# Kernel optimization log

Hardware: AMD Instinct MI355X
Metric: run time of the kernel (lower is better)

The kernel has to match this reference:

```python
import jax, jax.numpy as jnp
import numpy as np
from jax import lax

PATCH = 8

def setup_inputs() -> dict:
    key = jax.random.key(0)
    ks = jax.random.split(key, 5)
    x = jax.random.normal(ks[0], (4, 64, 256, 256), dtype=jnp.float32)
    w_in = jax.random.normal(ks[1], (512, 64), dtype=jnp.float32) * 0.02
    b_in = jnp.zeros((512,), dtype=jnp.float32)
    w_dw = jax.random.normal(ks[2], (512, 1, 3, 3), dtype=jnp.float32) * 0.02
    b_dw = jnp.zeros((512,), dtype=jnp.float32)
    w_out = jax.random.normal(ks[3], (64, 256), dtype=jnp.float32) * 0.02
    b_out = jnp.zeros((64,), dtype=jnp.float32)
    fft_filter = jnp.ones((64, 1, 1, PATCH, PATCH // 2 + 1), dtype=jnp.float32)
    return {"x": x, "w_in": w_in, "b_in": b_in, "w_dw": w_dw, "b_dw": b_dw,
            "w_out": w_out, "b_out": b_out, "fft_filter": fft_filter}

def reference(x, w_in, b_in, w_dw, b_dw, w_out, b_out, fft_filter):
    # project_in: 1x1 conv == channel GEMM. x: [B, C, H, W] -> [B, 2h, H, W]
    h = jnp.einsum('oc,bchw->bohw', w_in, x) + b_in[None, :, None, None]
    # depthwise 3x3 conv, padding=1
    h = lax.conv_general_dilated(
        h, w_dw, window_strides=(1, 1), padding='SAME',
        dimension_numbers=('NCHW', 'OIHW', 'NCHW'),
        feature_group_count=w_dw.shape[0]) + b_dw[None, :, None, None]
    x1, x2 = jnp.split(h, 2, axis=1)
    h = jax.nn.gelu(x1, approximate=False) * x2  # exact GELU like F.gelu
    # project_out: 1x1 conv
    y = jnp.einsum('oc,bchw->bohw', w_out, h) + b_out[None, :, None, None]
    # patch-wise spectral filtering
    B, C, H, W = y.shape
    p = PATCH
    yp = y.reshape(B, C, H // p, p, W // p, p).transpose(0, 1, 2, 4, 3, 5)  # b c h w p1 p2
    yf = jnp.fft.rfft2(yp)              # b c h w p1 (p2//2+1)
    yf = yf * fft_filter                # filter broadcasts over (c,1,1,p1,p2r)
    yp = jnp.fft.irfft2(yf, s=(p, p))
    y = yp.transpose(0, 1, 2, 4, 3, 5).reshape(B, C, H, W)
    return y
```

## Files before the change

### kernel.cpp

```cpp
#include <hip/hip_runtime.h>
#include <math.h>

typedef __attribute__((ext_vector_type(8))) short short8;
typedef __attribute__((ext_vector_type(4))) float f32x4;
typedef __attribute__((ext_vector_type(2))) float f32x2;
typedef _Float16 f16x8 __attribute__((ext_vector_type(8)));

#define TILE 16
#define IH 256
#define IW 256

#define WSA_OFF 16384
#define WSC_OFF 81920

#define H_STRIDE 1456
#define H_BUF 23296
#define G_OFF 46592
#define G_BUF 16384
#define SMEM_BYTES 79360

__device__ __forceinline__ unsigned short f2bf(float f) {
  unsigned int u = __builtin_bit_cast(unsigned int, f);
  u = (u + 0x7FFFu + ((u >> 16) & 1u)) >> 16;
  return (unsigned short)u;
}

__global__ void edffn_prep(const float* __restrict__ fftf,
                           const float* __restrict__ w_in,
                           const float* __restrict__ w_out,
                           float* __restrict__ ws) {
  int blk = blockIdx.x, t = threadIdx.x;
  if (blk < 64) {
    int a = t >> 3, bb = t & 7;
    const float c0 = 0.70710678118654752f;
    const float ctab[8] = {1.f, c0, 0.f, -c0, -1.f, -c0, 0.f, c0};
    const float* F = fftf + blk * 40;
    float acc = 0.f;
    for (int k1 = 0; k1 < 8; ++k1)
      for (int k2 = 0; k2 < 8; ++k2) {
        float f = (k2 <= 4) ? F[k1 * 5 + k2] : F[((8 - k1) & 7) * 5 + (8 - k2)];
        acc += f * ctab[(k1 * a + k2 * bb) & 7];
      }
    ws[blk * 64 + t] = acc * (1.f / 64.f);
  } else if (blk < 128) {
    int b2 = blk - 64;
    int q = b2 >> 2, s = (b2 >> 1) & 1, ks = b2 & 1;
    int row = (s ? 256 : 0) + q * 16 + (t & 15);
    unsigned short* dst =
        (unsigned short*)((unsigned char*)ws + WSA_OFF) + (((q * 2 + s) * 2 + ks) * 64 + t) * 8;
    for (int j = 0; j < 8; ++j) {
      int k = ks * 32 + (t >> 4) * 8 + j;
      dst[j] = f2bf(w_in[row * 64 + k]);
    }
  } else {
    int b3 = blk - 128;
    int p = b3 >> 2, mt = b3 & 3;
    int row = mt * 16 + (t & 15);
    unsigned short* dst =
        (unsigned short*)((unsigned char*)ws + WSC_OFF) + ((p * 4 + mt) * 64 + t) * 8;
    for (int j = 0; j < 8; ++j) {
      int k = p * 32 + (t >> 4) * 8 + j;
      _Float16 hv = (_Float16)w_out[row * 256 + k];
      dst[j] = __builtin_bit_cast(unsigned short, hv);
    }
  }
}

__global__ __launch_bounds__(256, 2) void edffn_main(
    const float* __restrict__ x, const float* __restrict__ b_in,
    const float* __restrict__ w_dw, const float* __restrict__ b_dw,
    const float* __restrict__ b_out, const float* __restrict__ ws,
    float* __restrict__ out) {
  __shared__ __align__(16) unsigned char smem[SMEM_BYTES];
  __shared__ int s_flag;
  const int t = threadIdx.x;
  const int lane = t & 63, wave = t >> 6;
  const int l15 = lane & 15, lg = lane >> 4;
  const int gx0 = blockIdx.x * TILE, gy0 = blockIdx.y * TILE;
  const int b = blockIdx.z;
  const unsigned short* wsA = (const unsigned short*)((const unsigned char*)ws + WSA_OFF);
  const unsigned short* wsC = (const unsigned short*)((const unsigned char*)ws + WSC_OFF);

  short8 xf[6][2];
  int haddr[6];
  unsigned vmask = 0, imask = 0;
  const float* xb = x + (size_t)b * 64 * 65536;
#pragma unroll
  for (int i = 0; i < 6; ++i) {
    int nt = wave + 4 * i;
    int n = nt * 16 + l15;
    int hy = n / 18;
    int hx = n - hy * 18;
    int gy = gy0 + hy - 1, gx = gx0 + hx - 1;
    int vnt = (nt < 21) & (n < 324);
    int inb = vnt & (gy >= 0) & (gy < IH) & (gx >= 0) & (gx < IW);
    haddr[i] = hy * 80 + hx * 4;
    vmask |= (unsigned)vnt << i;
    imask |= (unsigned)inb << i;
    int gyc = min(max(gy, 0), IH - 1), gxc = min(max(gx, 0), IW - 1);
    const float* xp = xb + (size_t)gyc * IW + gxc;
#pragma unroll
    for (int ks = 0; ks < 2; ++ks) {
#pragma unroll
      for (int j = 0; j < 8; ++j) {
        int k = ks * 32 + lg * 8 + j;
        unsigned short bf = f2bf(xp[(size_t)k * 65536]);
        xf[i][ks][j] = (short)(inb ? bf : (unsigned short)0);
      }
    }
  }

  f32x4 accY[16];
#pragma unroll
  for (int i = 0; i < 16; ++i) accY[i] = (f32x4){0.f, 0.f, 0.f, 0.f};

  const int cp_dw = t & 15;
  const int oy_dw = t >> 4;

  auto loadWD = [&](int qq, unsigned (&wd)[9], unsigned& bd) {
    const int cg1 = qq * 16 + cp_dw, cg2 = 256 + qq * 16 + cp_dw;
#pragma unroll
    for (int u = 0; u < 9; ++u) {
      float w1 = w_dw[cg1 * 9 + u], w2 = w_dw[cg2 * 9 + u];
      asm("v_cvt_pkrtz_f16_f32 %0, %1, %2" : "=v"(wd[u]) : "v"(w1), "v"(w2));
    }
    float b1 = b_dw[cg1], b2 = b_dw[cg2];
    asm("v_cvt_pkrtz_f16_f32 %0, %1, %2" : "=v"(bd) : "v"(b1), "v"(b2));
  };

  auto stageA = [&](int qq) {
    short8 af[2][2];
#pragma unroll
    for (int s = 0; s < 2; ++s)
#pragma unroll
      for (int ks = 0; ks < 2; ++ks)
        af[s][ks] = *(const short8*)(wsA + (((qq * 2 + s) * 2 + ks) * 64 + lane) * 8);
    float bin[2][4];
#pragma unroll
    for (int s = 0; s < 2; ++s)
#pragma unroll
      for (int r = 0; r < 4; ++r) bin[s][r] = b_in[(s ? 256 : 0) + qq * 16 + lg * 4 + r];
    unsigned char* Hb = smem + (qq & 1) * H_BUF;
#pragma unroll
    for (int i = 0; i < 6; ++i) {
      if (wave + 4 * i < 21) {
        f32x4 acc0 = {0.f, 0.f, 0.f, 0.f}, acc1 = {0.f, 0.f, 0.f, 0.f};
        acc0 = __builtin_amdgcn_mfma_f32_16x16x32_bf16(af[0][0], xf[i][0], acc0, 0, 0, 0);
        acc0 = __builtin_amdgcn_mfma_f32_16x16x32_bf16(af[0][1], xf[i][1], acc0, 0, 0, 0);
        acc1 = __builtin_amdgcn_mfma_f32_16x16x32_bf16(af[1][0], xf[i][0], acc1, 0, 0, 0);
        acc1 = __builtin_amdgcn_mfma_f32_16x16x32_bf16(af[1][1], xf[i][1], acc1, 0, 0, 0);
        if ((vmask >> i) & 1u) {
          unsigned keep = (imask >> i) & 1u;
#pragma unroll
          for (int r = 0; r < 4; ++r) {
            float v0 = acc0[r] + bin[0][r];
            float v1 = acc1[r] + bin[1][r];
            unsigned pk;
            asm("v_cvt_pkrtz_f16_f32 %0, %1, %2" : "=v"(pk) : "v"(v0), "v"(v1));
            pk = keep ? pk : 0u;
            *(unsigned*)(Hb + (lg * 4 + r) * H_STRIDE + haddr[i]) = pk;
          }
        }
      }
    }
  };

#define PKC(nm, val)                                            \
  unsigned nm;                                                  \
  {                                                             \
    float fv = (val);                                           \
    asm("v_cvt_pkrtz_f16_f32 %0, %1, %1" : "=v"(nm) : "v"(fv)); \
  }
  PKC(kSQ, 0.70710678f)
  PKC(kC216, 1.f / 216.f)
  PKC(kCm42, -1.f / 42.f)
  PKC(kC10, 0.1f)
  PKC(kCm3, -1.f / 3.f)
  PKC(kOne, 1.0f)
  PKC(kHalf, 0.5f)
  PKC(kErf, 1.12837917f)
#undef PKC

  auto dwconv = [&](int qq, const unsigned (&wd)[9], unsigned bd) {
    const int cp = cp_dw, oy = oy_dw;
    const unsigned char* Hb = smem + (qq & 1) * H_BUF;
    unsigned a[16];
#pragma unroll
    for (int j = 0; j < 16; ++j) a[j] = bd;
#pragma unroll
    for (int dy = 0; dy < 3; ++dy) {
      const uint4* rp = (const uint4*)(Hb + cp * H_STRIDE + (oy + dy) * 80);
      uint4 r0 = rp[0], r1 = rp[1], r2 = rp[2], r3 = rp[3];
      uint2 r4 = ((const uint2*)rp)[8];
      unsigned e[18] = {r0.x, r0.y, r0.z, r0.w, r1.x, r1.y, r1.z, r1.w,
                        r2.x, r2.y, r2.z, r2.w, r3.x, r3.y, r3.z, r3.w,
                        r4.x, r4.y};
#pragma unroll
      for (int ox = 0; ox < 16; ++ox) {
#pragma unroll
        for (int dx = 0; dx < 3; ++dx)
          asm("v_pk_fma_f16 %0, %1, %2, %0"
              : "+v"(a[ox])
              : "v"(wd[dy * 3 + dx]), "v"(e[ox + dx]));
      }
    }
    const int c2 = (qq & 1) * 16 + cp;
    const int gi = (c2 >> 3) ^ (oy & 3);
    unsigned short* Gp = (unsigned short*)(smem + G_OFF + ((qq >> 1) & 1) * G_BUF) +
                         oy * 16 * 32 + gi * 8 + (c2 & 7);
    unsigned umax = 0;
    unsigned gw[8];
#pragma unroll
    for (int j = 0; j < 8; ++j) {
      unsigned a0 = a[2 * j], a1 = a[2 * j + 1];
      unsigned u = __builtin_amdgcn_perm(a1, a0, 0x05040100u);
      unsigned v = __builtin_amdgcn_perm(a1, a0, 0x07060302u);
      unsigned uabs = u & 0x7FFF7FFFu;
      asm("v_pk_max_f16 %0, %1, %2" : "=v"(umax) : "v"(umax), "v"(uabs));
      unsigned z, z2, p, erfv, tt, g;
      asm("v_pk_mul_f16 %0, %1, %2" : "=v"(z) : "v"(u), "v"(kSQ));
      asm("v_pk_mul_f16 %0, %1, %2" : "=v"(z2) : "v"(z), "v"(z));
      asm("v_pk_fma_f16 %0, %1, %2, %3" : "=v"(p) : "v"(z2), "v"(kC216), "v"(kCm42));
      asm("v_pk_fma_f16 %0, %1, %2, %3" : "=v"(p) : "v"(z2), "v"(p), "v"(kC10));
      asm("v_pk_fma_f16 %0, %1, %2, %3" : "=v"(p) : "v"(z2), "v"(p), "v"(kCm3));
      asm("v_pk_fma_f16 %0, %1, %2, %3" : "=v"(p) : "v"(z2), "v"(p), "v"(kOne));
      asm("v_pk_mul_f16 %0, %1, %2" : "=v"(erfv) : "v"(z), "v"(p));
      asm("v_pk_mul_f16 %0, %1, %2" : "=v"(erfv) : "v"(erfv), "v"(kErf));
      asm("v_pk_fma_f16 %0, %1, %2, %2" : "=v"(tt) : "v"(erfv), "v"(kHalf));
      asm("v_pk_mul_f16 %0, %1, %2" : "=v"(g) : "v"(u), "v"(tt));
      asm("v_pk_mul_f16 %0, %1, %2" : "=v"(g) : "v"(g), "v"(v));
      gw[j] = g;
    }
    {
      float m0, m1;
      unsigned uh = umax >> 16;
      asm("v_cvt_f32_f16 %0, %1" : "=v"(m0) : "v"(umax));
      asm("v_cvt_f32_f16 %0, %1" : "=v"(m1) : "v"(uh));
      if (__builtin_expect(fmaxf(m0, m1) > 0.565685f, 0)) {
#pragma unroll
        for (int j = 0; j < 8; ++j) {
          float g01[2];
#pragma unroll
          for (int kx = 0; kx < 2; ++kx) {
            unsigned aw = a[2 * j + kx], ah = aw >> 16;
            float hu, hv2;
            asm("v_cvt_f32_f16 %0, %1" : "=v"(hu) : "v"(aw));
            asm("v_cvt_f32_f16 %0, %1" : "=v"(hv2) : "v"(ah));
            g01[kx] = 0.5f * hu * (1.f + erff(hu * 0.70710678f)) * hv2;
          }
          unsigned pk;
          asm("v_cvt_pkrtz_f16_f32 %0, %1, %2" : "=v"(pk) : "v"(g01[0]), "v"(g01[1]));
          gw[j] = pk;
        }
      }
    }
#pragma unroll
    for (int j = 0; j < 8; ++j) {
      Gp[(2 * j) * 32] = (unsigned short)gw[j];
      Gp[(2 * j + 1) * 32] = (unsigned short)(gw[j] >> 16);
    }
  };

  unsigned wdA[9], wdB[9], bdA, bdB;
  f16x8 cfC;

  auto stageC8 = [&](int pc, int nt0) {
    const unsigned short* G = (const unsigned short*)(smem + G_OFF + (pc & 1) * G_BUF);
#pragma unroll
    for (int k = 0; k < 8; ++k) {
      int nt = nt0 + k;
      int g = lg ^ (nt & 3);
      int n = nt * 16 + l15;
      f16x8 bf = *(const f16x8*)(G + n * 32 + g * 8);
      accY[nt] = __builtin_amdgcn_mfma_f32_16x16x32_f16(cfC, bf, accY[nt], 0, 0, 0);
    }
  };

  loadWD(0, wdA, bdA);
  loadWD(1, wdB, bdB);
  cfC = *(const f16x8*)(wsC + ((0 * 4 + wave) * 64 + lane) * 8);
  __builtin_amdgcn_s_setprio(1);
  stageA(0);
  stageA(1);
  __builtin_amdgcn_s_setprio(0);
  __syncthreads();

  for (int p = 0; p < 8; ++p) {
    if (p >= 1) {
      __builtin_amdgcn_s_setprio(1);
      stageC8(p - 1, 0);
      __builtin_amdgcn_s_setprio(0);
    }
    dwconv(2 * p, wdA, bdA);
    if (p >= 1) {
      __builtin_amdgcn_s_setprio(1);
      stageC8(p - 1, 8);
      __builtin_amdgcn_s_setprio(0);
      cfC = *(const f16x8*)(wsC + ((p * 4 + wave) * 64 + lane) * 8);
    }
    dwconv(2 * p + 1, wdB, bdB);
    __syncthreads();

    if (p < 7) {
      __builtin_amdgcn_s_setprio(1);
      stageA(2 * p + 2);
      stageA(2 * p + 3);
      __builtin_amdgcn_s_setprio(0);
      loadWD(2 * p + 2, wdA, bdA);
      loadWD(2 * p + 3, wdB, bdB);
      __syncthreads();
    }
  }

  __builtin_amdgcn_s_setprio(1);
  stageC8(7, 0);
  stageC8(7, 8);
  __builtin_amdgcn_s_setprio(0);

  {
    f32x4 bo;
#pragma unroll
    for (int r = 0; r < 4; ++r) bo[r] = b_out[wave * 16 + lg * 4 + r];
#pragma unroll
    for (int nt = 0; nt < 16; ++nt)
#pragma unroll
      for (int r = 0; r < 4; ++r) accY[nt][r] += bo[r];
  }

  if (t == 0) s_flag = 1;
  __syncthreads();
  {
    int ok = 1;
    const float* kc = ws;
#pragma unroll
    for (int j = 0; j < 16; ++j) {
      int idx = t * 16 + j;
      float e = ((idx & 63) == 0) ? 1.f : 0.f;
      ok &= (fabsf(kc[idx] - e) <= 1e-5f) ? 1 : 0;
    }
    if (!ok) s_flag = 0;
  }
  __syncthreads();

  const int o = wave * 16 + lg * 4;
  if (s_flag) {
#pragma unroll
    for (int nt = 0; nt < 16; ++nt) {
      float* op = out + (((size_t)(b * 64 + o)) * IH + gy0 + nt) * IW + gx0 + l15;
#pragma unroll
      for (int r = 0; r < 4; ++r) op[(size_t)r * IH * IW] = accY[nt][r];
    }
    return;
  }

  float* YS = (float*)smem;
  for (int half = 0; half < 2; ++half) {
    __syncthreads();
    if ((wave >> 1) == half) {
      int c32 = (wave & 1) * 16 + lg * 4;
#pragma unroll
      for (int nt = 0; nt < 16; ++nt)
#pragma unroll
        for (int r = 0; r < 4; ++r) YS[(c32 + r) * 260 + nt * 16 + l15] = accY[nt][r];
    }
    __syncthreads();
    if (t < 128) {
      int o32 = t >> 2, oo = half * 32 + o32, qd = t & 3;
      const float* kp = ws + oo * 64;
      int py0 = (qd >> 1) * 8, px0 = (qd & 1) * 8;
      const float* row = YS + o32 * 260;
      for (int i = 0; i < 8; ++i)
        for (int j = 0; j < 8; ++j) {
          float acc = 0.f;
          for (int a_ = 0; a_ < 8; ++a_)
            for (int b_ = 0; b_ < 8; ++b_)
              acc += kp[a_ * 8 + b_] *
                     row[(py0 + ((i - a_) & 7)) * 16 + px0 + ((j - b_) & 7)];
          out[(((size_t)(b * 64 + oo)) * IH + gy0 + py0 + i) * IW + gx0 + px0 + j] = acc;
        }
    }
  }
}

extern "C" void kernel_launch(void* const* d_in, const int* in_sizes, int n_in,
                              void* d_out, int out_size, void* d_ws, size_t ws_size,
                              hipStream_t stream) {
  const float* x = (const float*)d_in[0];
  const float* w_in = (const float*)d_in[1];
  const float* b_in = (const float*)d_in[2];
  const float* w_dw = (const float*)d_in[3];
  const float* b_dw = (const float*)d_in[4];
  const float* w_out = (const float*)d_in[5];
  const float* b_out = (const float*)d_in[6];
  const float* fftf = (const float*)d_in[7];
  float* out = (float*)d_out;
  float* ws = (float*)d_ws;

  edffn_prep<<<160, 64, 0, stream>>>(fftf, w_in, w_out, ws);
  dim3 grid(IW / TILE, IH / TILE, 4);
  edffn_main<<<grid, 256, 0, stream>>>(x, b_in, w_dw, b_dw, b_out, ws, out);
}
```

Measured before the change: 141.7 us.

## Split fused FFN kernel into two kernels with fp16 intermediate in workspace

Splits the single fused kernel into two. The first runs project-in, depthwise conv and GELU gating, then writes the gated fp16 activations to a global workspace buffer. The second reads them back with double-buffered LDS staging and runs project-out plus the spectral filter. The split lowers shared memory and register pressure per kernel so more blocks fit per CU. In exchange it adds a global round trip of about 134 MB of intermediate data and an extra launch, and falls back to the fused kernel if the workspace is too small.

```diff
diff --git a/kernel.cpp b/kernel.cpp
--- a/kernel.cpp
+++ b/kernel.cpp
@@ -12,12 +12,17 @@
 
 #define WSA_OFF 16384
 #define WSC_OFF 81920
+#define GH_OFF 131072
 
 #define H_STRIDE 1456
 #define H_BUF 23296
 #define G_OFF 46592
 #define G_BUF 16384
 #define SMEM_BYTES 79360
+
+#define K1_G_OFF 23296
+#define K1_SMEM 39680
+#define K2_SMEM 33280
 
 __device__ __forceinline__ unsigned short f2bf(float f) {
   unsigned int u = __builtin_bit_cast(unsigned int, f);
@@ -66,6 +71,13 @@
   }
 }
 
+#define PKC(nm, val)                                            \
+  unsigned nm;                                                  \
+  {                                                             \
+    float fv = (val);                                           \
+    asm("v_cvt_pkrtz_f16_f32 %0, %1, %1" : "=v"(nm) : "v"(fv)); \
+  }
+
 __global__ __launch_bounds__(256, 2) void edffn_main(
     const float* __restrict__ x, const float* __restrict__ b_in,
     const float* __restrict__ w_dw, const float* __restrict__ b_dw,
@@ -165,12 +177,6 @@
     }
   };
 
-#define PKC(nm, val)                                            \
-  unsigned nm;                                                  \
-  {                                                             \
-    float fv = (val);                                           \
-    asm("v_cvt_pkrtz_f16_f32 %0, %1, %1" : "=v"(nm) : "v"(fv)); \
-  }
   PKC(kSQ, 0.70710678f)
   PKC(kC216, 1.f / 216.f)
   PKC(kCm42, -1.f / 42.f)
@@ -179,7 +185,6 @@
   PKC(kOne, 1.0f)
   PKC(kHalf, 0.5f)
   PKC(kErf, 1.12837917f)
-#undef PKC
 
   auto dwconv = [&](int qq, const unsigned (&wd)[9], unsigned bd) {
     const int cp = cp_dw, oy = oy_dw;
@@ -300,7 +305,6 @@
     }
     dwconv(2 * p + 1, wdB, bdB);
     __syncthreads();
-
     if (p < 7) {
       __builtin_amdgcn_s_setprio(1);
       stageA(2 * p + 2);
@@ -382,6 +386,341 @@
   }
 }
 
+__global__ __launch_bounds__(256, 3) void edffn_k1(
+    const float* __restrict__ x, const float* __restrict__ b_in,
+    const float* __restrict__ w_dw, const float* __restrict__ b_dw,
+    const float* __restrict__ ws, unsigned char* __restrict__ Gh) {
+  __shared__ __align__(16) unsigned char smem[K1_SMEM];
+  const int t = threadIdx.x;
+  const int lane = t & 63, wave = t >> 6;
+  const int l15 = lane & 15, lg = lane >> 4;
+  const int gx0 = blockIdx.x * TILE, gy0 = blockIdx.y * TILE;
+  const int b = blockIdx.z;
+  const size_t blkL = ((size_t)b * 16 + blockIdx.y) * 16 + blockIdx.x;
+  const unsigned short* wsA = (const unsigned short*)((const unsigned char*)ws + WSA_OFF);
+
+  short8 xf[6][2];
+  int haddr[6];
+  unsigned vmask = 0, imask = 0;
+  const float* xb = x + (size_t)b * 64 * 65536;
+#pragma unroll
+  for (int i = 0; i < 6; ++i) {
+    int nt = wave + 4 * i;
+    int n = nt * 16 + l15;
+    int hy = n / 18;
+    int hx = n - hy * 18;
+    int gy = gy0 + hy - 1, gx = gx0 + hx - 1;
+    int vnt = (nt < 21) & (n < 324);
+    int inb = vnt & (gy >= 0) & (gy < IH) & (gx >= 0) & (gx < IW);
+    haddr[i] = hy * 80 + hx * 4;
+    vmask |= (unsigned)vnt << i;
+    imask |= (unsigned)inb << i;
+    int gyc = min(max(gy, 0), IH - 1), gxc = min(max(gx, 0), IW - 1);
+    const float* xp = xb + (size_t)gyc * IW + gxc;
+#pragma unroll
+    for (int ks = 0; ks < 2; ++ks) {
+#pragma unroll
+      for (int j = 0; j < 8; ++j) {
+        int k = ks * 32 + lg * 8 + j;
+        unsigned short bf = f2bf(xp[(size_t)k * 65536]);
+        xf[i][ks][j] = (short)(inb ? bf : (unsigned short)0);
+      }
+    }
+  }
+
+  const int cp_dw = t & 15;
+  const int oy_dw = t >> 4;
+
+  auto loadWD = [&](int qq, unsigned (&wd)[9], unsigned& bd) {
+    const int cg1 = qq * 16 + cp_dw, cg2 = 256 + qq * 16 + cp_dw;
+#pragma unroll
+    for (int u = 0; u < 9; ++u) {
+      float w1 = w_dw[cg1 * 9 + u], w2 = w_dw[cg2 * 9 + u];
+      asm("v_cvt_pkrtz_f16_f32 %0, %1, %2" : "=v"(wd[u]) : "v"(w1), "v"(w2));
+    }
+    float b1 = b_dw[cg1], b2 = b_dw[cg2];
+    asm("v_cvt_pkrtz_f16_f32 %0, %1, %2" : "=v"(bd) : "v"(b1), "v"(b2));
+  };
+
+  auto stageA = [&](int qq) {
+    short8 af[2][2];
+#pragma unroll
+    for (int s = 0; s < 2; ++s)
+#pragma unroll
+      for (int ks = 0; ks < 2; ++ks)
+        af[s][ks] = *(const short8*)(wsA + (((qq * 2 + s) * 2 + ks) * 64 + lane) * 8);
+    float bin[2][4];
+#pragma unroll
+    for (int s = 0; s < 2; ++s)
+#pragma unroll
+      for (int r = 0; r < 4; ++r) bin[s][r] = b_in[(s ? 256 : 0) + qq * 16 + lg * 4 + r];
+#pragma unroll
+    for (int i = 0; i < 6; ++i) {
+      if (wave + 4 * i < 21) {
+        f32x4 acc0 = {0.f, 0.f, 0.f, 0.f}, acc1 = {0.f, 0.f, 0.f, 0.f};
+        acc0 = __builtin_amdgcn_mfma_f32_16x16x32_bf16(af[0][0], xf[i][0], acc0, 0, 0, 0);
+        acc0 = __builtin_amdgcn_mfma_f32_16x16x32_bf16(af[0][1], xf[i][1], acc0, 0, 0, 0);
+        acc1 = __builtin_amdgcn_mfma_f32_16x16x32_bf16(af[1][0], xf[i][0], acc1, 0, 0, 0);
+        acc1 = __builtin_amdgcn_mfma_f32_16x16x32_bf16(af[1][1], xf[i][1], acc1, 0, 0, 0);
+        if ((vmask >> i) & 1u) {
+          unsigned keep = (imask >> i) & 1u;
+#pragma unroll
+          for (int r = 0; r < 4; ++r) {
+            float v0 = acc0[r] + bin[0][r];
+            float v1 = acc1[r] + bin[1][r];
+            unsigned pk;
+            asm("v_cvt_pkrtz_f16_f32 %0, %1, %2" : "=v"(pk) : "v"(v0), "v"(v1));
+            pk = keep ? pk : 0u;
+            *(unsigned*)(smem + (lg * 4 + r) * H_STRIDE + haddr[i]) = pk;
+          }
+        }
+      }
+    }
+  };
+
+  PKC(kSQ, 0.70710678f)
+  PKC(kC216, 1.f / 216.f)
+  PKC(kCm42, -1.f / 42.f)
+  PKC(kC10, 0.1f)
+  PKC(kCm3, -1.f / 3.f)
+  PKC(kOne, 1.0f)
+  PKC(kHalf, 0.5f)
+  PKC(kErf, 1.12837917f)
+
+  auto dwconv = [&](int qq, const unsigned (&wd)[9], unsigned bd) {
+    const int cp = cp_dw, oy = oy_dw;
+    unsigned a[16];
+#pragma unroll
+    for (int j = 0; j < 16; ++j) a[j] = bd;
+#pragma unroll
+    for (int dy = 0; dy < 3; ++dy) {
+      const uint4* rp = (const uint4*)(smem + cp * H_STRIDE + (oy + dy) * 80);
+      uint4 r0 = rp[0], r1 = rp[1], r2 = rp[2], r3 = rp[3];
+      uint2 r4 = ((const uint2*)rp)[8];
+      unsigned e[18] = {r0.x, r0.y, r0.z, r0.w, r1.x, r1.y, r1.z, r1.w,
+                        r2.x, r2.y, r2.z, r2.w, r3.x, r3.y, r3.z, r3.w,
+                        r4.x, r4.y};
+#pragma unroll
+      for (int ox = 0; ox < 16; ++ox) {
+#pragma unroll
+        for (int dx = 0; dx < 3; ++dx)
+          asm("v_pk_fma_f16 %0, %1, %2, %0"
+              : "+v"(a[ox])
+              : "v"(wd[dy * 3 + dx]), "v"(e[ox + dx]));
+      }
+    }
+    const int c2 = (qq & 1) * 16 + cp;
+    const int gi = (c2 >> 3) ^ (oy & 3);
+    unsigned short* Gp =
+        (unsigned short*)(smem + K1_G_OFF) + oy * 16 * 32 + gi * 8 + (c2 & 7);
+    unsigned umax = 0;
+    unsigned gw[8];
+#pragma unroll
+    for (int j = 0; j < 8; ++j) {
+      unsigned a0 = a[2 * j], a1 = a[2 * j + 1];
+      unsigned u = __builtin_amdgcn_perm(a1, a0, 0x05040100u);
+      unsigned v = __builtin_amdgcn_perm(a1, a0, 0x07060302u);
+      unsigned uabs = u & 0x7FFF7FFFu;
+      asm("v_pk_max_f16 %0, %1, %2" : "=v"(umax) : "v"(umax), "v"(uabs));
+      unsigned z, z2, p, erfv, tt, g;
+      asm("v_pk_mul_f16 %0, %1, %2" : "=v"(z) : "v"(u), "v"(kSQ));
+      asm("v_pk_mul_f16 %0, %1, %2" : "=v"(z2) : "v"(z), "v"(z));
+      asm("v_pk_fma_f16 %0, %1, %2, %3" : "=v"(p) : "v"(z2), "v"(kC216), "v"(kCm42));
+      asm("v_pk_fma_f16 %0, %1, %2, %3" : "=v"(p) : "v"(z2), "v"(p), "v"(kC10));
+      asm("v_pk_fma_f16 %0, %1, %2, %3" : "=v"(p) : "v"(z2), "v"(p), "v"(kCm3));
+      asm("v_pk_fma_f16 %0, %1, %2, %3" : "=v"(p) : "v"(z2), "v"(p), "v"(kOne));
+      asm("v_pk_mul_f16 %0, %1, %2" : "=v"(erfv) : "v"(z), "v"(p));
+      asm("v_pk_mul_f16 %0, %1, %2" : "=v"(erfv) : "v"(erfv), "v"(kErf));
+      asm("v_pk_fma_f16 %0, %1, %2, %2" : "=v"(tt) : "v"(erfv), "v"(kHalf));
+      asm("v_pk_mul_f16 %0, %1, %2" : "=v"(g) : "v"(u), "v"(tt));
+      asm("v_pk_mul_f16 %0, %1, %2" : "=v"(g) : "v"(g), "v"(v));
+      gw[j] = g;
+    }
+    {
+      float m0, m1;
+      unsigned uh = umax >> 16;
+      asm("v_cvt_f32_f16 %0, %1" : "=v"(m0) : "v"(umax));
+      asm("v_cvt_f32_f16 %0, %1" : "=v"(m1) : "v"(uh));
+      if (__builtin_expect(fmaxf(m0, m1) > 0.565685f, 0)) {
+#pragma unroll
+        for (int j = 0; j < 8; ++j) {
+          float g01[2];
+#pragma unroll
+          for (int kx = 0; kx < 2; ++kx) {
+            unsigned aw = a[2 * j + kx], ah = aw >> 16;
+            float hu, hv2;
+            asm("v_cvt_f32_f16 %0, %1" : "=v"(hu) : "v"(aw));
+            asm("v_cvt_f32_f16 %0, %1" : "=v"(hv2) : "v"(ah));
+            g01[kx] = 0.5f * hu * (1.f + erff(hu * 0.70710678f)) * hv2;
+          }
+          unsigned pk;
+          asm("v_cvt_pkrtz_f16_f32 %0, %1, %2" : "=v"(pk) : "v"(g01[0]), "v"(g01[1]));
+          gw[j] = pk;
+        }
+      }
+    }
+#pragma unroll
+    for (int j = 0; j < 8; ++j) {
+      Gp[(2 * j) * 32] = (unsigned short)gw[j];
+      Gp[(2 * j + 1) * 32] = (unsigned short)(gw[j] >> 16);
+    }
+  };
+
+  unsigned wd[9], bd;
+  for (int p8 = 0; p8 < 8; ++p8) {
+    loadWD(2 * p8, wd, bd);
+    __builtin_amdgcn_s_setprio(1);
+    stageA(2 * p8);
+    __builtin_amdgcn_s_setprio(0);
+    __syncthreads();
+    dwconv(2 * p8, wd, bd);
+    loadWD(2 * p8 + 1, wd, bd);
+    __syncthreads();
+    __builtin_amdgcn_s_setprio(1);
+    stageA(2 * p8 + 1);
+    __builtin_amdgcn_s_setprio(0);
+    __syncthreads();
+    dwconv(2 * p8 + 1, wd, bd);
+    __syncthreads();
+    {
+      int px = wave * 64 + (lane & 3) * 16 + ((lane >> 2) & 15);
+      const unsigned char* Gl = smem + K1_G_OFF;
+      int rr = (px >> 4) & 3;
+      uint4 v0 = *(const uint4*)(Gl + px * 64 + ((0 ^ rr)) * 16);
+      uint4 v1 = *(const uint4*)(Gl + px * 64 + ((1 ^ rr)) * 16);
+      uint4 v2 = *(const uint4*)(Gl + px * 64 + ((2 ^ rr)) * 16);
+      uint4 v3 = *(const uint4*)(Gl + px * 64 + ((3 ^ rr)) * 16);
+      uint4* dst = (uint4*)(Gh + ((blkL * 8 + p8) * 256 + px) * 64);
+      dst[0] = v0;
+      dst[1] = v1;
+      dst[2] = v2;
+      dst[3] = v3;
+    }
+    __syncthreads();
+  }
+}
+
+__global__ __launch_bounds__(256, 4) void edffn_k2(
+    const unsigned char* __restrict__ Gh, const float* __restrict__ ws,
+    const float* __restrict__ b_out, float* __restrict__ out) {
+  __shared__ __align__(16) unsigned char smem[K2_SMEM];
+  __shared__ int s_flag;
+  const int t = threadIdx.x;
+  const int lane = t & 63, wave = t >> 6;
+  const int l15 = lane & 15, lg = lane >> 4;
+  const int lgr = lg ^ ((l15 >> 1) & 3);
+  const int gx0 = blockIdx.x * TILE, gy0 = blockIdx.y * TILE;
+  const int b = blockIdx.z;
+  const size_t blkL = ((size_t)b * 16 + blockIdx.y) * 16 + blockIdx.x;
+  const unsigned short* wsC = (const unsigned short*)((const unsigned char*)ws + WSC_OFF);
+
+  f32x4 accY[16];
+#pragma unroll
+  for (int i = 0; i < 16; ++i) accY[i] = (f32x4){0.f, 0.f, 0.f, 0.f};
+
+  const int rr_w = ((t >> 4) ^ (t >> 1)) & 3;
+
+  auto loadGh = [&](int p, uint4 (&v)[4]) {
+    const uint4* src = (const uint4*)(Gh + ((blkL * 8 + p) * 256 + t) * 64);
+#pragma unroll
+    for (int g = 0; g < 4; ++g) v[g] = src[g];
+  };
+  auto stageWrite = [&](int buf, const uint4 (&v)[4]) {
+    unsigned char* L = smem + buf * 16384;
+#pragma unroll
+    for (int g = 0; g < 4; ++g) *(uint4*)(L + t * 64 + ((g ^ rr_w)) * 16) = v[g];
+  };
+
+  {
+    uint4 v[4];
+    loadGh(0, v);
+    stageWrite(0, v);
+  }
+  __syncthreads();
+
+  for (int p = 0; p < 8; ++p) {
+    uint4 v[4];
+    if (p < 7) loadGh(p + 1, v);
+    f16x8 cf = *(const f16x8*)(wsC + ((p * 4 + wave) * 64 + lane) * 8);
+    const unsigned char* L = smem + (p & 1) * 16384;
+    __builtin_amdgcn_s_setprio(1);
+#pragma unroll
+    for (int nt = 0; nt < 16; ++nt) {
+      int g = (lgr ^ nt) & 3;
+      int n = nt * 16 + l15;
+      f16x8 bf = *(const f16x8*)(L + n * 64 + g * 16);
+      accY[nt] = __builtin_amdgcn_mfma_f32_16x16x32_f16(cf, bf, accY[nt], 0, 0, 0);
+    }
+    __builtin_amdgcn_s_setprio(0);
+    if (p < 7) stageWrite((p + 1) & 1, v);
+    __syncthreads();
+  }
+
+  {
+    f32x4 bo;
+#pragma unroll
+    for (int r = 0; r < 4; ++r) bo[r] = b_out[wave * 16 + lg * 4 + r];
+#pragma unroll
+    for (int nt = 0; nt < 16; ++nt)
+#pragma unroll
+      for (int r = 0; r < 4; ++r) accY[nt][r] += bo[r];
+  }
+
+  if (t == 0) s_flag = 1;
+  __syncthreads();
+  {
+    int ok = 1;
+    const float* kc = ws;
+#pragma unroll
+    for (int j = 0; j < 16; ++j) {
+      int idx = t * 16 + j;
+      float e = ((idx & 63) == 0) ? 1.f : 0.f;
+      ok &= (fabsf(kc[idx] - e) <= 1e-5f) ? 1 : 0;
+    }
+    if (!ok) s_flag = 0;
+  }
+  __syncthreads();
+
+  const int o = wave * 16 + lg * 4;
+  if (s_flag) {
+#pragma unroll
+    for (int nt = 0; nt < 16; ++nt) {
+      float* op = out + (((size_t)(b * 64 + o)) * IH + gy0 + nt) * IW + gx0 + l15;
+#pragma unroll
+      for (int r = 0; r < 4; ++r) op[(size_t)r * IH * IW] = accY[nt][r];
+    }
+    return;
+  }
+
+  float* YS = (float*)smem;
+  for (int half = 0; half < 2; ++half) {
+    __syncthreads();
+    if ((wave >> 1) == half) {
+      int c32 = (wave & 1) * 16 + lg * 4;
+#pragma unroll
+      for (int nt = 0; nt < 16; ++nt)
+#pragma unroll
+        for (int r = 0; r < 4; ++r) YS[(c32 + r) * 260 + nt * 16 + l15] = accY[nt][r];
+    }
+    __syncthreads();
+    if (t < 128) {
+      int o32 = t >> 2, oo = half * 32 + o32, qd = t & 3;
+      const float* kp = ws + oo * 64;
+      int py0 = (qd >> 1) * 8, px0 = (qd & 1) * 8;
+      const float* row = YS + o32 * 260;
+      for (int i = 0; i < 8; ++i)
+        for (int j = 0; j < 8; ++j) {
+          float acc = 0.f;
+          for (int a_ = 0; a_ < 8; ++a_)
+            for (int b_ = 0; b_ < 8; ++b_)
+              acc += kp[a_ * 8 + b_] *
+                     row[(py0 + ((i - a_) & 7)) * 16 + px0 + ((j - b_) & 7)];
+          out[(((size_t)(b * 64 + oo)) * IH + gy0 + py0 + i) * IW + gx0 + px0 + j] = acc;
+        }
+    }
+  }
+}
+
 extern "C" void kernel_launch(void* const* d_in, const int* in_sizes, int n_in,
                               void* d_out, int out_size, void* d_ws, size_t ws_size,
                               hipStream_t stream) {
@@ -398,5 +737,12 @@
 
   edffn_prep<<<160, 64, 0, stream>>>(fftf, w_in, w_out, ws);
   dim3 grid(IW / TILE, IH / TILE, 4);
-  edffn_main<<<grid, 256, 0, stream>>>(x, b_in, w_dw, b_dw, b_out, ws, out);
+  const size_t NEED = (size_t)GH_OFF + (size_t)1024 * 8 * 256 * 64;
+  if (ws_size >= NEED) {
+    unsigned char* Gh = (unsigned char*)ws + GH_OFF;
+    edffn_k1<<<grid, 256, 0, stream>>>(x, b_in, w_dw, b_dw, ws, Gh);
+    edffn_k2<<<grid, 256, 0, stream>>>(Gh, ws, b_out, out);
+  } else {
+    edffn_main<<<grid, 256, 0, stream>>>(x, b_in, w_dw, b_dw, b_out, ws, out);
+  }
 }
```

After: 203.8 us. 1.44x slower.
